# Kernel optimization log

Hardware: AMD Instinct MI355X
Metric: run time of the kernel (lower is better)

Reference implementation:

```python
import jax, jax.numpy as jnp
import numpy as np

DIM = 512
HEADS = 8
DIM_HEAD = 64
INNER = HEADS * DIM_HEAD  # 512
EPS_LN = 1e-5
EPS_Q = 1e-6


def ternary_quant(w):
    # BitNet-style ternary quantization: scale by mean |w|, round to {-1,0,1}
    s = jnp.mean(jnp.abs(w))
    return jnp.round(jnp.clip(w / (s + EPS_Q), -1.0, 1.0)) * s


def layernorm(x, g, b):
    mu = jnp.mean(x, axis=-1, keepdims=True)
    var = jnp.mean(jnp.square(x - mu), axis=-1, keepdims=True)
    return (x - mu) * jax.lax.rsqrt(var + EPS_LN) * g + b


def setup_inputs() -> dict:
    key = jax.random.key(0)
    ks = jax.random.split(key, 6)
    x = jax.random.normal(ks[0], (8, 1024, DIM), dtype=jnp.float32)
    W_qkv = jax.random.normal(ks[1], (3 * INNER, DIM), dtype=jnp.float32) * (DIM ** -0.5)
    W_out = jax.random.normal(ks[2], (DIM, INNER), dtype=jnp.float32) * (INNER ** -0.5)
    b_out = jnp.zeros((DIM,), dtype=jnp.float32)
    g1 = jnp.ones((DIM,), dtype=jnp.float32)
    b1 = jnp.zeros((DIM,), dtype=jnp.float32)
    g2 = jnp.ones((INNER,), dtype=jnp.float32)
    b2 = jnp.zeros((INNER,), dtype=jnp.float32)
    return {"x": x, "g1": g1, "b1": b1, "W_qkv": W_qkv, "g2": g2, "b2": b2, "W_out": W_out, "b_out": b_out}


def reference(x, g1, b1, W_qkv, g2, b2, W_out, b_out):
    b, n, _ = x.shape
    scale = DIM_HEAD ** -0.5
    x = layernorm(x, g1, b1)
    qkv = x @ ternary_quant(W_qkv).T  # [b, n, 3*inner]
    q, k, v = jnp.split(qkv, 3, axis=-1)
    # b n (h d) -> b h n d
    def split_heads(t):
        return t.reshape(b, n, HEADS, DIM_HEAD).transpose(0, 2, 1, 3)
    q, k, v = split_heads(q), split_heads(k), split_heads(v)
    attn_map = jnp.einsum('bhnd,bhmd->bhnm', q, k) * scale  # [b,h,n,n]
    attn = jax.nn.softmax(attn_map, axis=-1)
    out = jnp.einsum('bhnm,bhmd->bhnd', attn, v)
    out = out.transpose(0, 2, 1, 3).reshape(b, n, INNER)  # b n (h d)
    out = layernorm(out, g2, b2)
    out = out @ ternary_quant(W_out).T + b_out
    return out
```

## Files before the change

### kernel.cpp

```cpp
#include <hip/hip_runtime.h>
#include <hip/hip_bf16.h>

typedef __bf16 bf16x8 __attribute__((ext_vector_type(8)));
typedef float  f32x4  __attribute__((ext_vector_type(4)));

#define SEQ   1024
#define BATCH 8
#define DIMM  512
#define HEADS 8
#define DHEAD 64
#define TRIPLE 1536
#define MROWS (BATCH*SEQ)

#define GLOAD_LDS16(g, l) __builtin_amdgcn_global_load_lds( \
    (const __attribute__((address_space(1))) void*)(const void*)(g), \
    (__attribute__((address_space(3))) void*)(void*)(l), 16, 0, 0)

__global__ void absum_partial(const float* __restrict__ w, int n, float* __restrict__ part) {
    __shared__ float red[4];
    float s = 0.f;
    for (int i = blockIdx.x * blockDim.x + threadIdx.x; i < n; i += gridDim.x * blockDim.x)
        s += fabsf(w[i]);
    for (int o = 32; o; o >>= 1) s += __shfl_down(s, o);
    int lane = threadIdx.x & 63, wv = threadIdx.x >> 6;
    if (!lane) red[wv] = s;
    __syncthreads();
    if (threadIdx.x == 0) {
        float t = red[0] + red[1] + red[2] + red[3];
        part[blockIdx.x] = t;
    }
}

__global__ void finalize_scales(const float* __restrict__ p1, const float* __restrict__ p2,
                                float* __restrict__ scales) {
    int t = threadIdx.x;
    float v1 = p1[t], v2 = p2[t];
    for (int o = 32; o; o >>= 1) { v1 += __shfl_down(v1, o); v2 += __shfl_down(v2, o); }
    __shared__ float r1[4], r2[4];
    int lane = t & 63, wv = t >> 6;
    if (!lane) { r1[wv] = v1; r2[wv] = v2; }
    __syncthreads();
    if (t == 0) {
        scales[0] = (r1[0] + r1[1] + r1[2] + r1[3]) / 786432.0f;
        scales[1] = (r2[0] + r2[1] + r2[2] + r2[3]) / 262144.0f;
    }
}

__global__ void quant_ternary(const float* __restrict__ w, int n,
                              const float* __restrict__ scp, int si,
                              __bf16* __restrict__ out) {
    float s = scp[si];
    float inv = 1.f / (s + 1e-6f);
    int idx = (blockIdx.x * blockDim.x + threadIdx.x) * 4;
    if (idx + 3 < n) {
        float4 v = *reinterpret_cast<const float4*>(w + idx);
        out[idx + 0] = (__bf16)(rintf(fminf(1.f, fmaxf(-1.f, v.x * inv))) * s);
        out[idx + 1] = (__bf16)(rintf(fminf(1.f, fmaxf(-1.f, v.y * inv))) * s);
        out[idx + 2] = (__bf16)(rintf(fminf(1.f, fmaxf(-1.f, v.z * inv))) * s);
        out[idx + 3] = (__bf16)(rintf(fminf(1.f, fmaxf(-1.f, v.w * inv))) * s);
    }
}

template<typename TIN>
__global__ __launch_bounds__(256) void ln_rows(const TIN* __restrict__ x,
                                               const float* __restrict__ g,
                                               const float* __restrict__ bta,
                                               __bf16* __restrict__ y) {
    int row = blockIdx.x;
    int t = threadIdx.x;
    const TIN* xr = x + (size_t)row * DIMM;
    float v0 = (float)xr[t * 2], v1 = (float)xr[t * 2 + 1];
    float s = v0 + v1, sq = v0 * v0 + v1 * v1;
    for (int o = 32; o; o >>= 1) { s += __shfl_down(s, o); sq += __shfl_down(sq, o); }
    __shared__ float rs[4], rq[4], mb[2];
    int lane = t & 63, wv = t >> 6;
    if (!lane) { rs[wv] = s; rq[wv] = sq; }
    __syncthreads();
    if (t == 0) {
        float S = rs[0] + rs[1] + rs[2] + rs[3];
        float Q = rq[0] + rq[1] + rq[2] + rq[3];
        float mu = S * (1.f / DIMM);
        float var = Q * (1.f / DIMM) - mu * mu;
        mb[0] = mu; mb[1] = rsqrtf(var + 1e-5f);
    }
    __syncthreads();
    float mu = mb[0], invs = mb[1];
    y[(size_t)row * DIMM + t * 2]     = (__bf16)((v0 - mu) * invs * g[t * 2]     + bta[t * 2]);
    y[(size_t)row * DIMM + t * 2 + 1] = (__bf16)((v1 - mu) * invs * g[t * 2 + 1] + bta[t * 2 + 1]);
}

template<int NCOLS, bool BIAS, bool OUT_F32>
__global__ __launch_bounds__(256) void gemm_lds(const __bf16* __restrict__ A,
                                                const __bf16* __restrict__ Wt,
                                                const float* __restrict__ bias,
                                                __bf16* __restrict__ outb,
                                                float* __restrict__ outf) {
    const int K = DIMM;
    __shared__ __align__(16) __bf16 As[128 * 32];
    __shared__ __align__(16) __bf16 Bs[128 * 32];

    const int tid = threadIdx.x;
    const int w = tid >> 6, lane = tid & 63;
    const int m = lane & 15, g = lane >> 4;
    const int mi = w >> 1, ni = w & 1;

    const int trow = tid >> 2;
    const int tc = tid & 3;
    const int sc = (tc ^ ((trow >> 1) & 3)) * 8;
    const __bf16* a0 = A  + (size_t)(blockIdx.x * 128 + trow) * K + sc;
    const __bf16* a1 = a0 + (size_t)64 * K;
    const __bf16* b0 = Wt + (size_t)(blockIdx.y * 128 + trow) * K + sc;
    const __bf16* b1 = b0 + (size_t)64 * K;
    char* lA0 = (char*)As + tid * 16;
    char* lA1 = (char*)As + 4096 + tid * 16;
    char* lB0 = (char*)Bs + tid * 16;
    char* lB1 = (char*)Bs + 4096 + tid * 16;

    f32x4 acc[4][4] = {};

    for (int k0 = 0; k0 < K; k0 += 32) {
        __syncthreads();
        GLOAD_LDS16(a0 + k0, lA0);
        GLOAD_LDS16(a1 + k0, lA1);
        GLOAD_LDS16(b0 + k0, lB0);
        GLOAD_LDS16(b1 + k0, lB1);
        __syncthreads();

        bf16x8 af[4], bfr[4];
#pragma unroll
        for (int i = 0; i < 4; ++i) {
            const int ra = mi * 64 + i * 16 + m;
            af[i] = *reinterpret_cast<const bf16x8*>(
                (const char*)As + ra * 64 + ((g ^ ((ra >> 1) & 3)) << 4));
        }
#pragma unroll
        for (int j = 0; j < 4; ++j) {
            const int rb = ni * 64 + j * 16 + m;
            bfr[j] = *reinterpret_cast<const bf16x8*>(
                (const char*)Bs + rb * 64 + ((g ^ ((rb >> 1) & 3)) << 4));
        }
#pragma unroll
        for (int i = 0; i < 4; ++i)
#pragma unroll
            for (int j = 0; j < 4; ++j)
                acc[i][j] = __builtin_amdgcn_mfma_f32_16x16x32_bf16(af[i], bfr[j], acc[i][j], 0, 0, 0);
    }

    const int orow0 = blockIdx.x * 128 + mi * 64 + g * 4;
    const int ocol0 = blockIdx.y * 128 + ni * 64;
#pragma unroll
    for (int i = 0; i < 4; ++i)
#pragma unroll
        for (int j = 0; j < 4; ++j)
#pragma unroll
            for (int r = 0; r < 4; ++r) {
                int row = orow0 + i * 16 + r;
                int col = ocol0 + j * 16 + m;
                float v = acc[i][j][r];
                if (BIAS) v += bias[col];
                if (OUT_F32) outf[(size_t)row * NCOLS + col] = v;
                else         outb[(size_t)row * NCOLS + col] = (__bf16)v;
            }
}

__global__ __launch_bounds__(256, 2) void attn_mfma(const __bf16* __restrict__ qkv,
                                                    __bf16* __restrict__ out) {
    const int qt = blockIdx.x, bh = blockIdx.y;
    const int b = bh >> 3, h = bh & 7;
    const int tid = threadIdx.x;
    const int w = tid >> 6, lane = tid & 63;
    const int g = lane >> 4, m = lane & 15;

    __shared__ __align__(16) __bf16 Kb[4096];
    __shared__ __align__(16) __bf16 Vt[4096];
    __shared__ __align__(16) __bf16 Pl[4][2048];

    bf16x8 qf[2][2];
    {
        const __bf16* qp = qkv + (size_t)(b * SEQ + qt * 128 + w * 32 + m) * TRIPLE + h * 64 + g * 8;
#pragma unroll
        for (int hf = 0; hf < 2; ++hf) {
            qf[hf][0] = *reinterpret_cast<const bf16x8*>(qp + (size_t)hf * 16 * TRIPLE);
            qf[hf][1] = *reinterpret_cast<const bf16x8*>(qp + (size_t)hf * 16 * TRIPLE + 32);
#pragma unroll
            for (int e = 0; e < 8; ++e) {
                qf[hf][0][e] = (__bf16)((float)qf[hf][0][e] * 0.125f);
                qf[hf][1][e] = (__bf16)((float)qf[hf][1][e] * 0.125f);
            }
        }
    }

    const int srow = tid >> 3;
    const int sc   = tid & 7;
    const size_t rbase = (size_t)(b * SEQ + srow) * TRIPLE + h * 64 + sc * 8;
    const __bf16* k0s = qkv + rbase + DIMM;
    const __bf16* v0s = qkv + rbase + 2 * DIMM;
    const __bf16* k1s = k0s + (size_t)32 * TRIPLE;
    const __bf16* v1s = v0s + (size_t)32 * TRIPLE;
    const int kstep = 64 * TRIPLE;

    char* kw0 = (char*)Kb + srow * 128 + ((sc ^ (srow & 7)) << 4);
    char* kw1 = kw0 + 32 * 128;
    char* vbp = (char*)Vt;

    f32x4 oa[2][4] = {};
    float mrun[2] = {-1e30f, -1e30f}, lrun[2] = {0.f, 0.f};

    uint4 k0c = *reinterpret_cast<const uint4*>(k0s);
    uint4 k1c = *reinterpret_cast<const uint4*>(k1s);
    uint4 v0c = *reinterpret_cast<const uint4*>(v0s);
    uint4 v1c = *reinterpret_cast<const uint4*>(v1s);
    uint4 k0n = {}, k1n = {}, v0n = {}, v1n = {};

    for (int t = 0; t < 16; ++t) {
        __syncthreads();

        *reinterpret_cast<bf16x8*>(kw0) = *reinterpret_cast<bf16x8*>(&k0c);
        *reinterpret_cast<bf16x8*>(kw1) = *reinterpret_cast<bf16x8*>(&k1c);
        {
            bf16x8 va = *reinterpret_cast<bf16x8*>(&v0c);
            bf16x8 vb = *reinterpret_cast<bf16x8*>(&v1c);
#pragma unroll
            for (int e = 0; e < 8; ++e) {
                const int dro = (sc * 8 + e) * 128;
                const int sw = ((sc ^ e) & 7) << 4;
                *(__bf16*)(vbp + dro + ((srow * 2) ^ sw))        = va[e];
                *(__bf16*)(vbp + dro + (((srow + 32) * 2) ^ sw)) = vb[e];
            }
        }
        __syncthreads();

        if (t < 15) {
            k0n = *reinterpret_cast<const uint4*>(k0s + (size_t)(t + 1) * kstep);
            k1n = *reinterpret_cast<const uint4*>(k1s + (size_t)(t + 1) * kstep);
            v0n = *reinterpret_cast<const uint4*>(v0s + (size_t)(t + 1) * kstep);
            v1n = *reinterpret_cast<const uint4*>(v1s + (size_t)(t + 1) * kstep);
        }

        const char* kb = (const char*)Kb;
        f32x4 sa[2][4];
#pragma unroll
        for (int hf = 0; hf < 2; ++hf)
#pragma unroll
            for (int i = 0; i < 4; ++i) sa[hf][i] = (f32x4){0.f, 0.f, 0.f, 0.f};
#pragma unroll
        for (int kc = 0; kc < 2; ++kc) {
            const int cp = ((kc * 4 + g) ^ (m & 7)) << 4;
#pragma unroll
            for (int i = 0; i < 4; ++i) {
                bf16x8 kf = *reinterpret_cast<const bf16x8*>(kb + (i * 16 + m) * 128 + cp);
                sa[0][i] = __builtin_amdgcn_mfma_f32_16x16x32_bf16(kf, qf[0][kc], sa[0][i], 0, 0, 0);
                sa[1][i] = __builtin_amdgcn_mfma_f32_16x16x32_bf16(kf, qf[1][kc], sa[1][i], 0, 0, 0);
            }
        }

        char* pw = (char*)Pl[w] + m * 128;
        const int psw = (m & 7) << 4;
#pragma unroll
        for (int hf = 0; hf < 2; ++hf) {
            float mx = -1e30f;
#pragma unroll
            for (int i = 0; i < 4; ++i)
#pragma unroll
                for (int r = 0; r < 4; ++r) mx = fmaxf(mx, sa[hf][i][r]);
            mx = fmaxf(mx, __shfl_xor(mx, 16));
            mx = fmaxf(mx, __shfl_xor(mx, 32));
            const float mnew = fmaxf(mrun[hf], mx);
            float p[4][4];
            float ps = 0.f;
#pragma unroll
            for (int i = 0; i < 4; ++i)
#pragma unroll
                for (int r = 0; r < 4; ++r) { p[i][r] = __expf(sa[hf][i][r] - mnew); ps += p[i][r]; }
            ps += __shfl_xor(ps, 16);
            ps += __shfl_xor(ps, 32);
            const float al = __expf(mrun[hf] - mnew);
            mrun[hf] = mnew;
            lrun[hf] = lrun[hf] * al + ps;
#pragma unroll
            for (int i = 0; i < 4; ++i)
#pragma unroll
                for (int r = 0; r < 4; ++r) oa[hf][i][r] *= al;
#pragma unroll
            for (int i = 0; i < 4; ++i) {
                uint2 pk;
                asm("v_cvt_pk_bf16_f32 %0, %1, %2" : "=v"(pk.x) : "v"(p[i][0]), "v"(p[i][1]));
                asm("v_cvt_pk_bf16_f32 %0, %1, %2" : "=v"(pk.y) : "v"(p[i][2]), "v"(p[i][3]));
                *reinterpret_cast<uint2*>(pw + hf * 16 * 128 + ((i * 32 + g * 8) ^ psw)) = pk;
            }
        }

        bf16x8 pf[2][2];
#pragma unroll
        for (int hf = 0; hf < 2; ++hf)
#pragma unroll
            for (int kc = 0; kc < 2; ++kc)
                pf[hf][kc] = *reinterpret_cast<const bf16x8*>(
                    pw + hf * 16 * 128 + ((kc * 64 + g * 16) ^ psw));

#pragma unroll
        for (int kc = 0; kc < 2; ++kc)
#pragma unroll
            for (int i = 0; i < 4; ++i) {
                const int sv = ((i * 2 + (m >> 3)) ^ (m & 7)) & 7;
                bf16x8 vf = *reinterpret_cast<const bf16x8*>(
                    vbp + (i * 16 + m) * 128 + (((kc * 4 + g) ^ sv) << 4));
                oa[0][i] = __builtin_amdgcn_mfma_f32_16x16x32_bf16(vf, pf[0][kc], oa[0][i], 0, 0, 0);
                oa[1][i] = __builtin_amdgcn_mfma_f32_16x16x32_bf16(vf, pf[1][kc], oa[1][i], 0, 0, 0);
            }

        k0c = k0n; k1c = k1n; v0c = v0n; v1c = v1n;
    }

#pragma unroll
    for (int hf = 0; hf < 2; ++hf) {
        const float inv = 1.0f / lrun[hf];
        unsigned int* orow = (unsigned int*)(out +
            (size_t)(b * SEQ + qt * 128 + w * 32 + hf * 16 + m) * DIMM + h * 64);
#pragma unroll
        for (int i = 0; i < 4; ++i)
#pragma unroll
            for (int rp = 0; rp < 2; ++rp) {
                float o0 = oa[hf][i][2 * rp] * inv, o1 = oa[hf][i][2 * rp + 1] * inv;
                unsigned int pk;
                asm("v_cvt_pk_bf16_f32 %0, %1, %2" : "=v"(pk) : "v"(o0), "v"(o1));
                orow[i * 8 + g * 2 + rp] = pk;
            }
    }
}

extern "C" void kernel_launch(void* const* d_in, const int* in_sizes, int n_in,
                              void* d_out, int out_size, void* d_ws, size_t ws_size,
                              hipStream_t stream) {
    const float* x     = (const float*)d_in[0];
    const float* g1    = (const float*)d_in[1];
    const float* b1    = (const float*)d_in[2];
    const float* W_qkv = (const float*)d_in[3];
    const float* g2    = (const float*)d_in[4];
    const float* b2    = (const float*)d_in[5];
    const float* W_out = (const float*)d_in[6];
    const float* b_out = (const float*)d_in[7];
    float* out = (float*)d_out;

    char* ws = (char*)d_ws;
    float* part1  = (float*)(ws);
    float* part2  = (float*)(ws + 1024);
    float* scales = (float*)(ws + 2048);
    __bf16* Wq1 = (__bf16*)(ws + 4096);
    __bf16* Wq2 = (__bf16*)(ws + 4096 + 1572864);
    __bf16* Xln = (__bf16*)(ws + 4096 + 1572864 + 524288);
    __bf16* QKV = (__bf16*)(ws + 4096 + 1572864 + 524288 + 8388608);
    __bf16* AO  = (__bf16*)(ws + 4096 + 1572864 + 524288 + 8388608 + 25165824);

    absum_partial<<<256, 256, 0, stream>>>(W_qkv, 786432, part1);
    absum_partial<<<256, 256, 0, stream>>>(W_out, 262144, part2);
    finalize_scales<<<1, 256, 0, stream>>>(part1, part2, scales);
    quant_ternary<<<768, 256, 0, stream>>>(W_qkv, 786432, scales, 0, Wq1);
    quant_ternary<<<256, 256, 0, stream>>>(W_out, 262144, scales, 1, Wq2);
    ln_rows<float><<<MROWS, 256, 0, stream>>>(x, g1, b1, Xln);
    gemm_lds<TRIPLE, false, false><<<dim3(64, 12), 256, 0, stream>>>(Xln, Wq1, nullptr, QKV, nullptr);
    attn_mfma<<<dim3(8, 64), 256, 0, stream>>>(QKV, AO);
    ln_rows<__bf16><<<MROWS, 256, 0, stream>>>(AO, g2, b2, Xln);
    gemm_lds<DIMM, true, true><<<dim3(64, 4), 256, 0, stream>>>(Xln, Wq2, b_out, nullptr, out);
}
```

Measured before the change: 103.7 us.

## Merge quantization launches, vectorize layernorm, double-buffer GEMM LDS loads

Combines the two absum reductions and the two ternary-quant kernels into single launches to cut launch overhead. Rewrites layernorm to process one row per wavefront with vectorized loads, xor-shuffle reduction and packed bf16 stores, removing shared-memory barriers. Adds LDS double buffering in the GEMM so the next K tile is prefetched while MFMAs run on the current one, at the cost of twice the LDS per block.

```diff
diff --git a/kernel.cpp b/kernel.cpp
--- a/kernel.cpp
+++ b/kernel.cpp
@@ -16,25 +16,35 @@
     (const __attribute__((address_space(1))) void*)(const void*)(g), \
     (__attribute__((address_space(3))) void*)(void*)(l), 16, 0, 0)
 
-__global__ void absum_partial(const float* __restrict__ w, int n, float* __restrict__ part) {
+__global__ __launch_bounds__(256) void absum_all(const float* __restrict__ w1,
+                                                 const float* __restrict__ w2,
+                                                 float* __restrict__ part) {
+    const int bid = blockIdx.x, tid = threadIdx.x;
+    float s = 0.f;
+    if (bid < 256) {
+        const float4* p = (const float4*)w1;
+        for (int i = bid * 256 + tid; i < 196608; i += 65536) {
+            float4 v = p[i];
+            s += fabsf(v.x) + fabsf(v.y) + fabsf(v.z) + fabsf(v.w);
+        }
+    } else {
+        const float4* p = (const float4*)w2;
+        for (int i = (bid - 256) * 256 + tid; i < 65536; i += 16384) {
+            float4 v = p[i];
+            s += fabsf(v.x) + fabsf(v.y) + fabsf(v.z) + fabsf(v.w);
+        }
+    }
+    for (int o = 32; o; o >>= 1) s += __shfl_down(s, o);
     __shared__ float red[4];
-    float s = 0.f;
-    for (int i = blockIdx.x * blockDim.x + threadIdx.x; i < n; i += gridDim.x * blockDim.x)
-        s += fabsf(w[i]);
-    for (int o = 32; o; o >>= 1) s += __shfl_down(s, o);
-    int lane = threadIdx.x & 63, wv = threadIdx.x >> 6;
-    if (!lane) red[wv] = s;
+    if (!(tid & 63)) red[tid >> 6] = s;
     __syncthreads();
-    if (threadIdx.x == 0) {
-        float t = red[0] + red[1] + red[2] + red[3];
-        part[blockIdx.x] = t;
-    }
-}
-
-__global__ void finalize_scales(const float* __restrict__ p1, const float* __restrict__ p2,
-                                float* __restrict__ scales) {
+    if (tid == 0) part[bid] = red[0] + red[1] + red[2] + red[3];
+}
+
+__global__ void finalize_scales(const float* __restrict__ part, float* __restrict__ scales) {
     int t = threadIdx.x;
-    float v1 = p1[t], v2 = p2[t];
+    float v1 = part[t];
+    float v2 = (t < 64) ? part[256 + t] : 0.f;
     for (int o = 32; o; o >>= 1) { v1 += __shfl_down(v1, o); v2 += __shfl_down(v2, o); }
     __shared__ float r1[4], r2[4];
     int lane = t & 63, wv = t >> 6;
@@ -46,47 +56,61 @@
     }
 }
 
-__global__ void quant_ternary(const float* __restrict__ w, int n,
-                              const float* __restrict__ scp, int si,
-                              __bf16* __restrict__ out) {
-    float s = scp[si];
-    float inv = 1.f / (s + 1e-6f);
-    int idx = (blockIdx.x * blockDim.x + threadIdx.x) * 4;
-    if (idx + 3 < n) {
-        float4 v = *reinterpret_cast<const float4*>(w + idx);
-        out[idx + 0] = (__bf16)(rintf(fminf(1.f, fmaxf(-1.f, v.x * inv))) * s);
-        out[idx + 1] = (__bf16)(rintf(fminf(1.f, fmaxf(-1.f, v.y * inv))) * s);
-        out[idx + 2] = (__bf16)(rintf(fminf(1.f, fmaxf(-1.f, v.z * inv))) * s);
-        out[idx + 3] = (__bf16)(rintf(fminf(1.f, fmaxf(-1.f, v.w * inv))) * s);
-    }
+__global__ __launch_bounds__(256) void quant_all(const float* __restrict__ w1,
+                                                 const float* __restrict__ w2,
+                                                 const float* __restrict__ scp,
+                                                 __bf16* __restrict__ o1,
+                                                 __bf16* __restrict__ o2) {
+    const int bid = blockIdx.x;
+    const float* w; __bf16* o; float s; int idx;
+    if (bid < 768) { w = w1; o = o1; s = scp[0]; idx = (bid * 256 + threadIdx.x) * 4; }
+    else           { w = w2; o = o2; s = scp[1]; idx = ((bid - 768) * 256 + threadIdx.x) * 4; }
+    const float inv = 1.f / (s + 1e-6f);
+    float4 v = *reinterpret_cast<const float4*>(w + idx);
+    o[idx + 0] = (__bf16)(rintf(fminf(1.f, fmaxf(-1.f, v.x * inv))) * s);
+    o[idx + 1] = (__bf16)(rintf(fminf(1.f, fmaxf(-1.f, v.y * inv))) * s);
+    o[idx + 2] = (__bf16)(rintf(fminf(1.f, fmaxf(-1.f, v.z * inv))) * s);
+    o[idx + 3] = (__bf16)(rintf(fminf(1.f, fmaxf(-1.f, v.w * inv))) * s);
 }
 
 template<typename TIN>
-__global__ __launch_bounds__(256) void ln_rows(const TIN* __restrict__ x,
+__global__ __launch_bounds__(256) void ln_fast(const TIN* __restrict__ x,
                                                const float* __restrict__ g,
                                                const float* __restrict__ bta,
                                                __bf16* __restrict__ y) {
-    int row = blockIdx.x;
-    int t = threadIdx.x;
-    const TIN* xr = x + (size_t)row * DIMM;
-    float v0 = (float)xr[t * 2], v1 = (float)xr[t * 2 + 1];
-    float s = v0 + v1, sq = v0 * v0 + v1 * v1;
-    for (int o = 32; o; o >>= 1) { s += __shfl_down(s, o); sq += __shfl_down(sq, o); }
-    __shared__ float rs[4], rq[4], mb[2];
-    int lane = t & 63, wv = t >> 6;
-    if (!lane) { rs[wv] = s; rq[wv] = sq; }
-    __syncthreads();
-    if (t == 0) {
-        float S = rs[0] + rs[1] + rs[2] + rs[3];
-        float Q = rq[0] + rq[1] + rq[2] + rq[3];
-        float mu = S * (1.f / DIMM);
-        float var = Q * (1.f / DIMM) - mu * mu;
-        mb[0] = mu; mb[1] = rsqrtf(var + 1e-5f);
-    }
-    __syncthreads();
-    float mu = mb[0], invs = mb[1];
-    y[(size_t)row * DIMM + t * 2]     = (__bf16)((v0 - mu) * invs * g[t * 2]     + bta[t * 2]);
-    y[(size_t)row * DIMM + t * 2 + 1] = (__bf16)((v1 - mu) * invs * g[t * 2 + 1] + bta[t * 2 + 1]);
+    const int row = blockIdx.x * 4 + (threadIdx.x >> 6);
+    const int lane = threadIdx.x & 63;
+    float v[8];
+    if constexpr (sizeof(TIN) == 4) {
+        const float4* xr = (const float4*)((const float*)x + (size_t)row * DIMM + lane * 8);
+        float4 a = xr[0], bq = xr[1];
+        v[0] = a.x; v[1] = a.y; v[2] = a.z; v[3] = a.w;
+        v[4] = bq.x; v[5] = bq.y; v[6] = bq.z; v[7] = bq.w;
+    } else {
+        bf16x8 a = *reinterpret_cast<const bf16x8*>((const __bf16*)x + (size_t)row * DIMM + lane * 8);
+#pragma unroll
+        for (int e = 0; e < 8; ++e) v[e] = (float)a[e];
+    }
+    float s = 0.f, sq = 0.f;
+#pragma unroll
+    for (int e = 0; e < 8; ++e) { s += v[e]; sq += v[e] * v[e]; }
+    for (int o = 32; o; o >>= 1) { s += __shfl_xor(s, o); sq += __shfl_xor(sq, o); }
+    const float mu = s * (1.f / DIMM);
+    const float invs = rsqrtf(sq * (1.f / DIMM) - mu * mu + 1e-5f);
+    const float4* gp = (const float4*)(g + lane * 8);
+    const float4* bp = (const float4*)(bta + lane * 8);
+    float4 g0 = gp[0], g1 = gp[1], b0 = bp[0], b1 = bp[1];
+    float o_[8] = {
+        (v[0] - mu) * invs * g0.x + b0.x, (v[1] - mu) * invs * g0.y + b0.y,
+        (v[2] - mu) * invs * g0.z + b0.z, (v[3] - mu) * invs * g0.w + b0.w,
+        (v[4] - mu) * invs * g1.x + b1.x, (v[5] - mu) * invs * g1.y + b1.y,
+        (v[6] - mu) * invs * g1.z + b1.z, (v[7] - mu) * invs * g1.w + b1.w };
+    uint4 st;
+    asm("v_cvt_pk_bf16_f32 %0, %1, %2" : "=v"(st.x) : "v"(o_[0]), "v"(o_[1]));
+    asm("v_cvt_pk_bf16_f32 %0, %1, %2" : "=v"(st.y) : "v"(o_[2]), "v"(o_[3]));
+    asm("v_cvt_pk_bf16_f32 %0, %1, %2" : "=v"(st.z) : "v"(o_[4]), "v"(o_[5]));
+    asm("v_cvt_pk_bf16_f32 %0, %1, %2" : "=v"(st.w) : "v"(o_[6]), "v"(o_[7]));
+    *reinterpret_cast<uint4*>(y + (size_t)row * DIMM + lane * 8) = st;
 }
 
 template<int NCOLS, bool BIAS, bool OUT_F32>
@@ -96,8 +120,8 @@
                                                 __bf16* __restrict__ outb,
                                                 float* __restrict__ outf) {
     const int K = DIMM;
-    __shared__ __align__(16) __bf16 As[128 * 32];
-    __shared__ __align__(16) __bf16 Bs[128 * 32];
+    __shared__ __align__(16) __bf16 As[2][4096];
+    __shared__ __align__(16) __bf16 Bs[2][4096];
 
     const int tid = threadIdx.x;
     const int w = tid >> 6, lane = tid & 63;
@@ -111,39 +135,43 @@
     const __bf16* a1 = a0 + (size_t)64 * K;
     const __bf16* b0 = Wt + (size_t)(blockIdx.y * 128 + trow) * K + sc;
     const __bf16* b1 = b0 + (size_t)64 * K;
-    char* lA0 = (char*)As + tid * 16;
-    char* lA1 = (char*)As + 4096 + tid * 16;
-    char* lB0 = (char*)Bs + tid * 16;
-    char* lB1 = (char*)Bs + 4096 + tid * 16;
 
     f32x4 acc[4][4] = {};
 
+    GLOAD_LDS16(a0, (char*)As[0] + tid * 16);
+    GLOAD_LDS16(a1, (char*)As[0] + 4096 + tid * 16);
+    GLOAD_LDS16(b0, (char*)Bs[0] + tid * 16);
+    GLOAD_LDS16(b1, (char*)Bs[0] + 4096 + tid * 16);
+
+    int cur = 0;
     for (int k0 = 0; k0 < K; k0 += 32) {
         __syncthreads();
-        GLOAD_LDS16(a0 + k0, lA0);
-        GLOAD_LDS16(a1 + k0, lA1);
-        GLOAD_LDS16(b0 + k0, lB0);
-        GLOAD_LDS16(b1 + k0, lB1);
-        __syncthreads();
-
+        if (k0 + 32 < K) {
+            GLOAD_LDS16(a0 + k0 + 32, (char*)As[cur ^ 1] + tid * 16);
+            GLOAD_LDS16(a1 + k0 + 32, (char*)As[cur ^ 1] + 4096 + tid * 16);
+            GLOAD_LDS16(b0 + k0 + 32, (char*)Bs[cur ^ 1] + tid * 16);
+            GLOAD_LDS16(b1 + k0 + 32, (char*)Bs[cur ^ 1] + 4096 + tid * 16);
+        }
+
+        const char* Ab = (const char*)As[cur];
+        const char* Bb = (const char*)Bs[cur];
         bf16x8 af[4], bfr[4];
 #pragma unroll
         for (int i = 0; i < 4; ++i) {
             const int ra = mi * 64 + i * 16 + m;
-            af[i] = *reinterpret_cast<const bf16x8*>(
-                (const char*)As + ra * 64 + ((g ^ ((ra >> 1) & 3)) << 4));
+            af[i] = *reinterpret_cast<const bf16x8*>(Ab + ra * 64 + ((g ^ ((ra >> 1) & 3)) << 4));
         }
 #pragma unroll
         for (int j = 0; j < 4; ++j) {
             const int rb = ni * 64 + j * 16 + m;
-            bfr[j] = *reinterpret_cast<const bf16x8*>(
-                (const char*)Bs + rb * 64 + ((g ^ ((rb >> 1) & 3)) << 4));
+            bfr[j] = *reinterpret_cast<const bf16x8*>(Bb + rb * 64 + ((g ^ ((rb >> 1) & 3)) << 4));
         }
 #pragma unroll
         for (int i = 0; i < 4; ++i)
 #pragma unroll
             for (int j = 0; j < 4; ++j)
                 acc[i][j] = __builtin_amdgcn_mfma_f32_16x16x32_bf16(af[i], bfr[j], acc[i][j], 0, 0, 0);
+        cur ^= 1;
     }
 
     const int orow0 = blockIdx.x * 128 + mi * 64 + g * 4;
@@ -343,8 +371,7 @@
     float* out = (float*)d_out;
 
     char* ws = (char*)d_ws;
-    float* part1  = (float*)(ws);
-    float* part2  = (float*)(ws + 1024);
+    float* part   = (float*)(ws);
     float* scales = (float*)(ws + 2048);
     __bf16* Wq1 = (__bf16*)(ws + 4096);
     __bf16* Wq2 = (__bf16*)(ws + 4096 + 1572864);
@@ -352,14 +379,12 @@
     __bf16* QKV = (__bf16*)(ws + 4096 + 1572864 + 524288 + 8388608);
     __bf16* AO  = (__bf16*)(ws + 4096 + 1572864 + 524288 + 8388608 + 25165824);
 
-    absum_partial<<<256, 256, 0, stream>>>(W_qkv, 786432, part1);
-    absum_partial<<<256, 256, 0, stream>>>(W_out, 262144, part2);
-    finalize_scales<<<1, 256, 0, stream>>>(part1, part2, scales);
-    quant_ternary<<<768, 256, 0, stream>>>(W_qkv, 786432, scales, 0, Wq1);
-    quant_ternary<<<256, 256, 0, stream>>>(W_out, 262144, scales, 1, Wq2);
-    ln_rows<float><<<MROWS, 256, 0, stream>>>(x, g1, b1, Xln);
+    absum_all<<<320, 256, 0, stream>>>(W_qkv, W_out, part);
+    finalize_scales<<<1, 256, 0, stream>>>(part, scales);
+    quant_all<<<1024, 256, 0, stream>>>(W_qkv, W_out, scales, Wq1, Wq2);
+    ln_fast<float><<<MROWS / 4, 256, 0, stream>>>(x, g1, b1, Xln);
     gemm_lds<TRIPLE, false, false><<<dim3(64, 12), 256, 0, stream>>>(Xln, Wq1, nullptr, QKV, nullptr);
     attn_mfma<<<dim3(8, 64), 256, 0, stream>>>(QKV, AO);
-    ln_rows<__bf16><<<MROWS, 256, 0, stream>>>(AO, g2, b2, Xln);
+    ln_fast<__bf16><<<MROWS / 4, 256, 0, stream>>>(AO, g2, b2, Xln);
     gemm_lds<DIMM, true, true><<<dim3(64, 4), 256, 0, stream>>>(Xln, Wq2, b_out, nullptr, out);
 }
```

New measurement: 90.40 us. 1.15x faster.
